# Optimization experiments

Hardware: AMD Instinct MI355X
Metric: run time of the kernel (lower is better)

Reference implementation:

```python
import jax, jax.numpy as jnp
import numpy as np

N, E, IN_DIM, HID, HEADS = 50000, 400000, 128, 64, 4
NEG_SLOPE, LN_EPS = 0.2, 1e-5


def setup_inputs() -> dict:
    key = jax.random.key(0)
    ks = jax.random.split(key, 12)
    x = jax.random.normal(ks[0], (N, IN_DIM), dtype=jnp.float32)
    edge_index = jax.random.randint(ks[1], (2, E), 0, N, dtype=jnp.int64)
    s = 1.0 / np.sqrt(HID)
    return {
        "x": x,
        "edge_index": edge_index,
        "W_gcn": jax.random.normal(ks[2], (IN_DIM, HID), dtype=jnp.float32) / np.sqrt(IN_DIM),
        "b_gcn": jnp.zeros((HID,), dtype=jnp.float32),
        "W_gat": jax.random.normal(ks[3], (HID, HEADS * HID), dtype=jnp.float32) * s,
        "att_src": jax.random.normal(ks[4], (HEADS, HID), dtype=jnp.float32) * s,
        "att_dst": jax.random.normal(ks[5], (HEADS, HID), dtype=jnp.float32) * s,
        "b_gat": jnp.zeros((HID,), dtype=jnp.float32),
        "W_patch": jax.random.normal(ks[6], (HID, HID), dtype=jnp.float32) * s,
        "b_patch": jnp.zeros((HID,), dtype=jnp.float32),
        "gamma": jnp.ones((HID,), dtype=jnp.float32),
        "beta": jnp.zeros((HID,), dtype=jnp.float32),
    }


def _forward(x, edge_index, W_gcn, b_gcn, W_gat, att_src, att_dst, b_gat,
             W_patch, b_patch, gamma, beta):
    n = x.shape[0]
    loop = jnp.arange(n, dtype=edge_index.dtype)
    src = jnp.concatenate([edge_index[0], loop])  # self-loops appended (PyG default)
    dst = jnp.concatenate([edge_index[1], loop])

    # ---- GCNConv: symmetric degree normalization + scatter-add ----
    deg = jax.ops.segment_sum(jnp.ones_like(dst, dtype=jnp.float32), dst, num_segments=n)
    dinv = jnp.where(deg > 0, jax.lax.rsqrt(deg), 0.0)
    norm = dinv[src] * dinv[dst]  # [E+N]
    xw = x @ W_gcn  # [N,HID]
    h1 = jax.ops.segment_sum(xw[src] * norm[:, None], dst, num_segments=n) + b_gcn
    h1 = jax.nn.relu(h1)

    # ---- GATConv (heads=4, concat=False -> mean over heads) ----
    z = (h1 @ W_gat).reshape(n, HEADS, HID)  # [N,H,C]
    a_s = jnp.einsum('nhc,hc->nh', z, att_src)  # [N,H]
    a_d = jnp.einsum('nhc,hc->nh', z, att_dst)
    e = jax.nn.leaky_relu(a_s[src] + a_d[dst], negative_slope=NEG_SLOPE)  # [E+N,H]
    # segment-softmax over incoming edges per destination node
    m = jax.ops.segment_max(e, dst, num_segments=n)  # [N,H]
    ex = jnp.exp(e - m[dst])
    denom = jax.ops.segment_sum(ex, dst, num_segments=n)
    alpha = ex / denom[dst]  # [E+N,H]
    agg = jax.ops.segment_sum(z[src] * alpha[:, :, None], dst, num_segments=n)  # [N,H,C]
    h2 = jax.nn.relu(agg.mean(axis=1) + b_gat)

    # ---- residual fusion + LayerNorm (dropout is identity in eval) ----
    h_patch = h1 @ W_patch + b_patch
    h = h1 + h2 + h_patch
    mu = h.mean(axis=-1, keepdims=True)
    var = h.var(axis=-1, keepdims=True)
    return (h - mu) * jax.lax.rsqrt(var + LN_EPS) * gamma + beta


def reference(x, edge_index, W_gcn, b_gcn, W_gat, att_src, att_dst, b_gat,
              W_patch, b_patch, gamma, beta):
    return _forward(x, edge_index, W_gcn, b_gcn, W_gat, att_src, att_dst, b_gat,
                    W_patch, b_patch, gamma, beta)
```

## Files before the change

kernel.cpp:

```cpp
#include <hip/hip_runtime.h>
#include <math.h>

#define IN_DIM 128
#define HID 64
#define HEADS 4
#define NEG_SLOPE 0.2f
#define LN_EPS 1e-5f
#define ECAP 512

typedef short bf16x8 __attribute__((ext_vector_type(8)));
typedef float f32x4  __attribute__((ext_vector_type(4)));

__device__ inline unsigned short f2bf(float f) {
    unsigned u = __float_as_uint(f);
    u += 0x7fffu + ((u >> 16) & 1u);
    return (unsigned short)(u >> 16);
}
__device__ inline float bf2f(unsigned short s) {
    return __uint_as_float(((unsigned)s) << 16);
}
__device__ inline float leaky(float v) { return v > 0.0f ? v : NEG_SLOPE * v; }

__global__ void k_init_all(const unsigned long long* ei, int E, int n,
                           int* flag, int* hist,
                           const float* __restrict__ Wg, const float* __restrict__ Wp,
                           const float* __restrict__ Wgcn,
                           const float* __restrict__ att_s, const float* __restrict__ att_d,
                           unsigned short* __restrict__ Wt_post,
                           unsigned short* __restrict__ Wt_xw,
                           float* __restrict__ w_s, float* __restrict__ w_d) {
    int nzb = (n + 255) >> 8;
    int t = threadIdx.x;
    if ((int)blockIdx.x < nzb) {
        int i = blockIdx.x * 256 + t;
        if (i < n) hist[i] = 0;
        if (blockIdx.x == 0) {
            __shared__ int s_bad;
            if (t == 0) s_bad = 0;
            __syncthreads();
            int lim = E < 4096 ? E : 4096;
            int bad = 0;
            for (int k = t; k < lim; k += 256)
                if (ei[k] >= (unsigned long long)n) bad = 1;
            if (bad) s_bad = 1;
            __syncthreads();
            if (t == 0) *flag = s_bad ? 0 : 1;
        }
        return;
    }
    int role = blockIdx.x - nzb;
    if (role < 14) {
        int p = role * 256 + t;
        if (p < 2560) {
            int c = p & 63, kg = p >> 6;
            bf16x8 v;
#pragma unroll
            for (int j = 0; j < 8; j++) {
                int k = kg * 8 + j;
                float f;
                if (k < 256) f = 0.25f * Wg[(size_t)(k & 63) * 256 + (k >> 6) * 64 + c];
                else         f = Wp[(size_t)(k - 256) * 64 + c];
                v[j] = (short)f2bf(f);
            }
            *(bf16x8*)(&Wt_post[(size_t)p * 8]) = v;
        } else if (p < 2560 + 1024) {
            int q = p - 2560;
            int c = q & 63, kg = q >> 6;
            bf16x8 v;
#pragma unroll
            for (int j = 0; j < 8; j++)
                v[j] = (short)f2bf(Wgcn[(size_t)(kg * 8 + j) * 64 + c]);
            *(bf16x8*)(&Wt_xw[(size_t)q * 8]) = v;
        }
    } else {
        int h = t >> 6, k = t & 63;
        float ss = 0.0f, sd = 0.0f;
        for (int c = 0; c < HID; c++) {
            float w = Wg[(size_t)k * (HEADS * HID) + h * HID + c];
            ss += w * att_s[h * HID + c];
            sd += w * att_d[h * HID + c];
        }
        w_s[h * HID + k] = ss;
        w_d[h * HID + k] = sd;
    }
}

__global__ void k_hist(const void* ei, int E, const int* flag, int* hist) {
    int i = blockIdx.x * blockDim.x + threadIdx.x;
    if (i >= E) return;
    int is64 = *flag;
    int d;
    if (is64) d = (int)((const long long*)ei)[E + i];
    else      d = ((const int*)ei)[E + i];
    atomicAdd(&hist[d], 1);
}

__global__ __launch_bounds__(256) void k_scan1(const int* __restrict__ hist,
                                               int* __restrict__ tmp,
                                               int* __restrict__ partial, int n) {
    __shared__ int s[256];
    int t = threadIdx.x, i = blockIdx.x * 256 + t;
    int v = (i < n) ? hist[i] : 0;
    s[t] = v;
    __syncthreads();
    for (int off = 1; off < 256; off <<= 1) {
        int x = (t >= off) ? s[t - off] : 0;
        __syncthreads();
        s[t] += x;
        __syncthreads();
    }
    tmp[i] = s[t] - v;
    if (t == 255) partial[blockIdx.x] = s[255];
}

__global__ __launch_bounds__(256) void k_scan_apply(const int* __restrict__ tmp,
                                                    const int* __restrict__ partial,
                                                    const int* __restrict__ hist,
                                                    int* __restrict__ row_ptr,
                                                    int* __restrict__ cursor,
                                                    float* __restrict__ dinv,
                                                    int n, int nscan) {
    __shared__ int s[256];
    __shared__ int excl_s;
    int t = threadIdx.x;
    int v = (t < nscan) ? partial[t] : 0;
    s[t] = v;
    __syncthreads();
    for (int off = 1; off < 256; off <<= 1) {
        int x = (t >= off) ? s[t - off] : 0;
        __syncthreads();
        s[t] += x;
        __syncthreads();
    }
    if (t == 0) excl_s = (blockIdx.x == 0) ? 0 : s[blockIdx.x - 1];
    __syncthreads();
    int excl = excl_s;
    int i = blockIdx.x * 256 + t;
    if (i < n) {
        int v2 = tmp[i] + excl;
        row_ptr[i] = v2;
        cursor[i] = v2;
        dinv[i] = rsqrtf((float)(hist[i] + 1));
    }
}

__global__ __launch_bounds__(256) void k_scatter_xw(const void* ei, int E,
                                                    const int* __restrict__ flag,
                                                    int* __restrict__ cursor,
                                                    int* __restrict__ col,
                                                    const float* __restrict__ x,
                                                    const unsigned short* __restrict__ Wt_g,
                                                    const float* __restrict__ dinv,
                                                    unsigned short* __restrict__ xws, int n) {
    __shared__ unsigned short Wt[16 * 64 * 8];
    int nsb = (E + 255) >> 8;
    if ((int)blockIdx.x < nsb) {
        int i = blockIdx.x * 256 + threadIdx.x;
        if (i >= E) return;
        int is64 = *flag;
        int s, d;
        if (is64) { s = (int)((const long long*)ei)[i]; d = (int)((const long long*)ei)[E + i]; }
        else      { s = ((const int*)ei)[i];            d = ((const int*)ei)[E + i]; }
        int pos = atomicAdd(&cursor[d], 1);
        col[pos] = s;
    } else {
        int bx = blockIdx.x - nsb;
        int t = threadIdx.x;
        for (int idx = t; idx < 1024; idx += 256)
            *(bf16x8*)(&Wt[idx * 8]) = *(const bf16x8*)(&Wt_g[(size_t)idx * 8]);
        __syncthreads();
        int lane = t & 63;
        int li = lane & 15, quad = lane >> 4;
        int w = t >> 6;
        int r0 = bx * 64 + w * 16;
        int rload = r0 + li; if (rload > n - 1) rload = n - 1;
        f32x4 acc[4];
#pragma unroll
        for (int i = 0; i < 4; i++) acc[i] = (f32x4){0.f, 0.f, 0.f, 0.f};
        const float* xp = x + (size_t)rload * IN_DIM + quad * 8;
#pragma unroll
        for (int ks = 0; ks < 4; ks++) {
            float4 p0 = *(const float4*)(xp + ks * 32);
            float4 p1 = *(const float4*)(xp + ks * 32 + 4);
            bf16x8 a;
            a[0] = (short)f2bf(p0.x); a[1] = (short)f2bf(p0.y);
            a[2] = (short)f2bf(p0.z); a[3] = (short)f2bf(p0.w);
            a[4] = (short)f2bf(p1.x); a[5] = (short)f2bf(p1.y);
            a[6] = (short)f2bf(p1.z); a[7] = (short)f2bf(p1.w);
            int kg = ks * 4 + quad;
#pragma unroll
            for (int tt = 0; tt < 4; tt++) {
                bf16x8 bfr = *(const bf16x8*)(&Wt[((kg * 64) + tt * 16 + li) * 8]);
                acc[tt] = __builtin_amdgcn_mfma_f32_16x16x32_bf16(a, bfr, acc[tt], 0, 0, 0);
            }
        }
#pragma unroll
        for (int reg = 0; reg < 4; reg++) {
            int r = r0 + quad * 4 + reg;
            if (r >= n) continue;
            float dv = dinv[r];
#pragma unroll
            for (int tt = 0; tt < 4; tt++)
                xws[(size_t)r * HID + tt * 16 + li] = f2bf(acc[tt][reg] * dv);
        }
    }
}

__global__ __launch_bounds__(256) void k_gcn(const int* __restrict__ col,
                                             const int* __restrict__ row_ptr,
                                             const int* __restrict__ hist,
                                             const float* __restrict__ dinv,
                                             const unsigned short* __restrict__ xws,
                                             const float* __restrict__ b,
                                             const float* __restrict__ w_s,
                                             const float* __restrict__ w_d,
                                             unsigned short* __restrict__ h1b,
                                             float4* __restrict__ a_s,
                                             float4* __restrict__ a_d, int n) {
    int t = threadIdx.x, c = t & 63;
    int d = blockIdx.x * 4 + (t >> 6);
    if (d >= n) return;
    int start = row_ptr[d], cnt = hist[d];
    float acc = bf2f(xws[(size_t)d * HID + c]);
    int k = 0;
    for (; k + 3 < cnt; k += 4) {
        int s0 = col[start + k],     s1 = col[start + k + 1];
        int s2 = col[start + k + 2], s3 = col[start + k + 3];
        float v0 = bf2f(xws[(size_t)s0 * HID + c]);
        float v1 = bf2f(xws[(size_t)s1 * HID + c]);
        float v2 = bf2f(xws[(size_t)s2 * HID + c]);
        float v3 = bf2f(xws[(size_t)s3 * HID + c]);
        acc += (v0 + v1) + (v2 + v3);
    }
    for (; k < cnt; k++) acc += bf2f(xws[(size_t)col[start + k] * HID + c]);
    float h1c = fmaxf(acc * dinv[d] + b[c], 0.0f);
    h1b[(size_t)d * HID + c] = f2bf(h1c);
    float vs0 = h1c * w_s[c],       vs1 = h1c * w_s[64 + c];
    float vs2 = h1c * w_s[128 + c], vs3 = h1c * w_s[192 + c];
    float vd0 = h1c * w_d[c],       vd1 = h1c * w_d[64 + c];
    float vd2 = h1c * w_d[128 + c], vd3 = h1c * w_d[192 + c];
    for (int o = 32; o > 0; o >>= 1) {
        vs0 += __shfl_xor(vs0, o, 64); vs1 += __shfl_xor(vs1, o, 64);
        vs2 += __shfl_xor(vs2, o, 64); vs3 += __shfl_xor(vs3, o, 64);
        vd0 += __shfl_xor(vd0, o, 64); vd1 += __shfl_xor(vd1, o, 64);
        vd2 += __shfl_xor(vd2, o, 64); vd3 += __shfl_xor(vd3, o, 64);
    }
    if (c == 0) {
        a_s[d] = make_float4(vs0, vs1, vs2, vs3);
        a_d[d] = make_float4(vd0, vd1, vd2, vd3);
    }
}

__global__ __launch_bounds__(256) void k_attn(const int* __restrict__ col,
                                              const int* __restrict__ row_ptr,
                                              const int* __restrict__ hist,
                                              const float4* __restrict__ a_s,
                                              const float4* __restrict__ a_d,
                                              const unsigned short* __restrict__ h1b,
                                              unsigned short* __restrict__ X, int n) {
    __shared__ float4 wls[ECAP];
    __shared__ int    sls[ECAP];
    __shared__ int    sb[5];
    __shared__ float4 sad[4];
    int t = threadIdx.x;
    int d0 = blockIdx.x * 4;
    if (t == 0) {
        int bptr = row_ptr[d0];
        sb[0] = bptr;
        for (int j = 0; j < 4; j++) {
            int d = d0 + j;
            bptr += (d < n) ? hist[d] : 0;
            sb[j + 1] = bptr;
        }
    }
    if (t < 4 && d0 + t < n) sad[t] = a_d[d0 + t];
    __syncthreads();
    int start0 = sb[0];
    int totc = sb[4] - start0;
    int rel1 = sb[1] - start0, rel2 = sb[2] - start0, rel3 = sb[3] - start0;
    bool fast = (totc <= ECAP);
    if (fast) {
        for (int e = t; e < totc; e += 256) {
            int s = col[start0 + e];
            int j = (e >= rel1) + (e >= rel2) + (e >= rel3);
            float4 as = a_s[s], ad = sad[j];
            float4 w;
            w.x = __expf(leaky(as.x + ad.x));
            w.y = __expf(leaky(as.y + ad.y));
            w.z = __expf(leaky(as.z + ad.z));
            w.w = __expf(leaky(as.w + ad.w));
            wls[e] = w;
            sls[e] = s;
        }
    }
    __syncthreads();
    int c = t & 63, w = t >> 6;
    int d = d0 + w;
    if (d >= n) return;
    float4 ad = sad[w];
    float4 asd = a_s[d];
    float w0 = __expf(leaky(asd.x + ad.x));
    float w1 = __expf(leaky(asd.y + ad.y));
    float w2 = __expf(leaky(asd.z + ad.z));
    float w3 = __expf(leaky(asd.w + ad.w));
    float hs = bf2f(h1b[(size_t)d * HID + c]);
    float A0 = w0 * hs, A1 = w1 * hs, A2 = w2 * hs, A3 = w3 * hs;
    float l0 = w0, l1 = w1, l2 = w2, l3 = w3;
    int lo = sb[w] - start0, hi = sb[w + 1] - start0;
    if (fast) {
        int k = lo;
        for (; k + 3 < hi; k += 4) {
            int s0 = sls[k], s1 = sls[k + 1], s2 = sls[k + 2], s3 = sls[k + 3];
            float4 e0 = wls[k], e1 = wls[k + 1], e2 = wls[k + 2], e3 = wls[k + 3];
            float hv0 = bf2f(h1b[(size_t)s0 * HID + c]);
            float hv1 = bf2f(h1b[(size_t)s1 * HID + c]);
            float hv2 = bf2f(h1b[(size_t)s2 * HID + c]);
            float hv3 = bf2f(h1b[(size_t)s3 * HID + c]);
            A0 += e0.x * hv0 + e1.x * hv1 + e2.x * hv2 + e3.x * hv3;
            A1 += e0.y * hv0 + e1.y * hv1 + e2.y * hv2 + e3.y * hv3;
            A2 += e0.z * hv0 + e1.z * hv1 + e2.z * hv2 + e3.z * hv3;
            A3 += e0.w * hv0 + e1.w * hv1 + e2.w * hv2 + e3.w * hv3;
            l0 += (e0.x + e1.x) + (e2.x + e3.x);
            l1 += (e0.y + e1.y) + (e2.y + e3.y);
            l2 += (e0.z + e1.z) + (e2.z + e3.z);
            l3 += (e0.w + e1.w) + (e2.w + e3.w);
        }
        for (; k < hi; k++) {
            int s0 = sls[k];
            float4 e0 = wls[k];
            float hv0 = bf2f(h1b[(size_t)s0 * HID + c]);
            A0 += e0.x * hv0; l0 += e0.x;
            A1 += e0.y * hv0; l1 += e0.y;
            A2 += e0.z * hv0; l2 += e0.z;
            A3 += e0.w * hv0; l3 += e0.w;
        }
    } else {
        for (int k = lo; k < hi; k++) {
            int s0 = col[start0 + k];
            float4 as = a_s[s0];
            float u0 = __expf(leaky(as.x + ad.x));
            float u1 = __expf(leaky(as.y + ad.y));
            float u2 = __expf(leaky(as.z + ad.z));
            float u3 = __expf(leaky(as.w + ad.w));
            float hv0 = bf2f(h1b[(size_t)s0 * HID + c]);
            A0 += u0 * hv0; l0 += u0;
            A1 += u1 * hv0; l1 += u1;
            A2 += u2 * hv0; l2 += u2;
            A3 += u3 * hv0; l3 += u3;
        }
    }
    size_t base = (size_t)d * 256;
    X[base + c]       = f2bf(A0 / l0);
    X[base + 64 + c]  = f2bf(A1 / l1);
    X[base + 128 + c] = f2bf(A2 / l2);
    X[base + 192 + c] = f2bf(A3 / l3);
}

__global__ __launch_bounds__(256) void k_post(const unsigned short* __restrict__ Wt_g,
                                              const unsigned short* __restrict__ X,
                                              const unsigned short* __restrict__ h1b,
                                              const float* __restrict__ bp,
                                              const float* __restrict__ bg,
                                              const float* __restrict__ gamma,
                                              const float* __restrict__ beta,
                                              float* __restrict__ out, int n) {
    __shared__ unsigned short Wt[2560 * 8];
    int t = threadIdx.x;
    for (int idx = t; idx < 2560; idx += 256)
        *(bf16x8*)(&Wt[idx * 8]) = *(const bf16x8*)(&Wt_g[(size_t)idx * 8]);
    __syncthreads();

    int lane = t & 63;
    int li = lane & 15, quad = lane >> 4;
    int w = t >> 6;
    int rbase = blockIdx.x * 128 + w * 32;

    f32x4 acc_a[2][4], acc_h[2][4];
#pragma unroll
    for (int rt = 0; rt < 2; rt++)
#pragma unroll
        for (int i = 0; i < 4; i++) {
            acc_a[rt][i] = (f32x4){0.f, 0.f, 0.f, 0.f};
            acc_h[rt][i] = (f32x4){0.f, 0.f, 0.f, 0.f};
        }
#pragma unroll
    for (int ks = 0; ks < 10; ks++) {
        int kg = ks * 4 + quad;
        bf16x8 b0 = *(const bf16x8*)(&Wt[((kg * 64) + 0 * 16 + li) * 8]);
        bf16x8 b1 = *(const bf16x8*)(&Wt[((kg * 64) + 1 * 16 + li) * 8]);
        bf16x8 b2 = *(const bf16x8*)(&Wt[((kg * 64) + 2 * 16 + li) * 8]);
        bf16x8 b3 = *(const bf16x8*)(&Wt[((kg * 64) + 3 * 16 + li) * 8]);
#pragma unroll
        for (int rt = 0; rt < 2; rt++) {
            int row = rbase + rt * 16 + li;
            bf16x8 a;
            if (ks < 8)
                a = *(const bf16x8*)(X + (size_t)row * 256 + quad * 8 + ks * 32);
            else
                a = *(const bf16x8*)(h1b + (size_t)row * HID + quad * 8 + (ks - 8) * 32);
            if (ks < 8) {
                acc_a[rt][0] = __builtin_amdgcn_mfma_f32_16x16x32_bf16(a, b0, acc_a[rt][0], 0, 0, 0);
                acc_a[rt][1] = __builtin_amdgcn_mfma_f32_16x16x32_bf16(a, b1, acc_a[rt][1], 0, 0, 0);
                acc_a[rt][2] = __builtin_amdgcn_mfma_f32_16x16x32_bf16(a, b2, acc_a[rt][2], 0, 0, 0);
                acc_a[rt][3] = __builtin_amdgcn_mfma_f32_16x16x32_bf16(a, b3, acc_a[rt][3], 0, 0, 0);
            } else {
                acc_h[rt][0] = __builtin_amdgcn_mfma_f32_16x16x32_bf16(a, b0, acc_h[rt][0], 0, 0, 0);
                acc_h[rt][1] = __builtin_amdgcn_mfma_f32_16x16x32_bf16(a, b1, acc_h[rt][1], 0, 0, 0);
                acc_h[rt][2] = __builtin_amdgcn_mfma_f32_16x16x32_bf16(a, b2, acc_h[rt][2], 0, 0, 0);
                acc_h[rt][3] = __builtin_amdgcn_mfma_f32_16x16x32_bf16(a, b3, acc_h[rt][3], 0, 0, 0);
            }
        }
    }
    float bgv[4], bpv[4], gv[4], btv[4];
#pragma unroll
    for (int tt = 0; tt < 4; tt++) {
        int c = tt * 16 + li;
        bgv[tt] = bg[c]; bpv[tt] = bp[c]; gv[tt] = gamma[c]; btv[tt] = beta[c];
    }
#pragma unroll
    for (int rt = 0; rt < 2; rt++) {
#pragma unroll
        for (int reg = 0; reg < 4; reg++) {
            int r = rbase + rt * 16 + quad * 4 + reg;
            bool ok = (r < n);
            float hv[4];
            float s1 = 0.0f, s2 = 0.0f;
#pragma unroll
            for (int tt = 0; tt < 4; tt++) {
                int c = tt * 16 + li;
                float h1c = ok ? bf2f(h1b[(size_t)r * HID + c]) : 0.0f;
                float h2 = fmaxf(acc_a[rt][tt][reg] + bgv[tt], 0.0f);
                float h = h1c + h2 + acc_h[rt][tt][reg] + bpv[tt];
                hv[tt] = h;
                s1 += h; s2 += h * h;
            }
            for (int o = 8; o > 0; o >>= 1) {
                s1 += __shfl_xor(s1, o, 64);
                s2 += __shfl_xor(s2, o, 64);
            }
            float mu = s1 * (1.0f / 64.0f);
            float var = s2 * (1.0f / 64.0f) - mu * mu;
            float rs = rsqrtf(var + LN_EPS);
            if (ok) {
#pragma unroll
                for (int tt = 0; tt < 4; tt++) {
                    int c = tt * 16 + li;
                    out[(size_t)r * HID + c] = (hv[tt] - mu) * rs * gv[tt] + btv[tt];
                }
            }
        }
    }
}

extern "C" void kernel_launch(void* const* d_in, const int* in_sizes, int n_in,
                              void* d_out, int out_size, void* d_ws, size_t ws_size,
                              hipStream_t stream) {
    int n = in_sizes[0] / IN_DIM;
    int E = in_sizes[1] / 2;

    const float* x     = (const float*)d_in[0];
    const void*  ei    = d_in[1];
    const float* W_gcn = (const float*)d_in[2];
    const float* b_gcn = (const float*)d_in[3];
    const float* W_gat = (const float*)d_in[4];
    const float* att_s = (const float*)d_in[5];
    const float* att_d = (const float*)d_in[6];
    const float* b_gat = (const float*)d_in[7];
    const float* W_p   = (const float*)d_in[8];
    const float* b_p   = (const float*)d_in[9];
    const float* gamma = (const float*)d_in[10];
    const float* beta  = (const float*)d_in[11];

    int n_pad  = ((n + 255) / 256) * 256;
    int nscan  = n_pad / 256;
    int n128   = ((n + 127) / 128) * 128;
    int nzb    = (n + 255) / 256;
    int nsb    = (E + 255) / 256;

    float* ws = (float*)d_ws;
    size_t off = 0;
    int*   flag    = (int*)(ws + off);  off += 4;
    int*   hist    = (int*)(ws + off);  off += n;
    int*   row_ptr = (int*)(ws + off);  off += n;
    int*   cursor  = (int*)(ws + off);  off += n;
    int*   tmp     = (int*)(ws + off);  off += n_pad;
    int*   partial = (int*)(ws + off);  off += 256;
    int*   colv    = (int*)(ws + off);  off += E;
    float* dinv    = ws + off;          off += n;
    float* w_s     = ws + off;          off += HEADS * HID;
    float* w_d     = ws + off;          off += HEADS * HID;
    off = (off + 3) & ~(size_t)3;
    unsigned short* Wt_post = (unsigned short*)(ws + off); off += 2560 * 8 / 2;
    unsigned short* Wt_xw   = (unsigned short*)(ws + off); off += 1024 * 8 / 2;
    unsigned short* xws = (unsigned short*)(ws + off); off += (size_t)n * HID / 2;
    off = (off + 3) & ~(size_t)3;
    unsigned short* h1b = (unsigned short*)(ws + off); off += (size_t)n128 * HID / 2;
    off = (off + 3) & ~(size_t)3;
    float4* a_sv   = (float4*)(ws + off); off += (size_t)n * 4;
    float4* a_dv   = (float4*)(ws + off); off += (size_t)n * 4;
    off = (off + 3) & ~(size_t)3;
    unsigned short* X = (unsigned short*)(ws + off); off += (size_t)n128 * 256 / 2;

    k_init_all<<<nzb + 15, 256, 0, stream>>>((const unsigned long long*)ei, E, n,
                                             flag, hist, W_gat, W_p, W_gcn,
                                             att_s, att_d, Wt_post, Wt_xw, w_s, w_d);
    k_hist<<<nsb, 256, 0, stream>>>(ei, E, flag, hist);

    k_scan1<<<nscan, 256, 0, stream>>>(hist, tmp, partial, n);
    k_scan_apply<<<nscan, 256, 0, stream>>>(tmp, partial, hist, row_ptr, cursor,
                                            dinv, n, nscan);

    k_scatter_xw<<<nsb + (n + 63) / 64, 256, 0, stream>>>(ei, E, flag, cursor,
                                                          colv, x, Wt_xw,
                                                          dinv, xws, n);

    k_gcn<<<(n + 3) / 4, 256, 0, stream>>>(colv, row_ptr, hist, dinv, xws, b_gcn,
                                           w_s, w_d, h1b, a_sv, a_dv, n);

    k_attn<<<(n + 3) / 4, 256, 0, stream>>>(colv, row_ptr, hist, a_sv, a_dv,
                                            h1b, X, n);

    k_post<<<(n + 127) / 128, 256, 0, stream>>>(Wt_post, X, h1b, b_p, b_gat,
                                                gamma, beta, (float*)d_out, n);
}
```

Baseline: 225.2 us.

## Fuse GAT attention aggregation with post-projection MFMA and LayerNorm

Merges the attention-aggregation and post-processing kernels into one. Each block aggregates 16 destination rows into a shared-memory bf16 tile, then runs the MFMA projection and LayerNorm directly from that tile, so the 256-wide intermediate X never goes through global memory. The GCN and attention gathers are restructured so each lane loads 4 contiguous bf16 values and the four 16-lane quarters of a wave walk different edges, combined with cross-quarter shuffles. The trade-offs are that attention weights are recomputed per edge instead of staged in shared memory, and the weight tile is read from global memory per block rather than cached in LDS.

```diff
diff --git a/kernel.cpp b/kernel.cpp
--- a/kernel.cpp
+++ b/kernel.cpp
@@ -6,10 +6,11 @@
 #define HEADS 4
 #define NEG_SLOPE 0.2f
 #define LN_EPS 1e-5f
-#define ECAP 512
+#define APAD 328
 
 typedef short bf16x8 __attribute__((ext_vector_type(8)));
 typedef float f32x4  __attribute__((ext_vector_type(4)));
+typedef unsigned short u16x4 __attribute__((ext_vector_type(4)));
 
 __device__ inline unsigned short f2bf(float f) {
     unsigned u = __float_as_uint(f);
@@ -217,238 +218,203 @@
                                              unsigned short* __restrict__ h1b,
                                              float4* __restrict__ a_s,
                                              float4* __restrict__ a_d, int n) {
-    int t = threadIdx.x, c = t & 63;
-    int d = blockIdx.x * 4 + (t >> 6);
+    int t = threadIdx.x;
+    int w = t >> 6, lane = t & 63, q = lane >> 4, li = lane & 15;
+    int d = blockIdx.x * 4 + w;
     if (d >= n) return;
     int start = row_ptr[d], cnt = hist[d];
-    float acc = bf2f(xws[(size_t)d * HID + c]);
-    int k = 0;
-    for (; k + 3 < cnt; k += 4) {
-        int s0 = col[start + k],     s1 = col[start + k + 1];
-        int s2 = col[start + k + 2], s3 = col[start + k + 3];
-        float v0 = bf2f(xws[(size_t)s0 * HID + c]);
-        float v1 = bf2f(xws[(size_t)s1 * HID + c]);
-        float v2 = bf2f(xws[(size_t)s2 * HID + c]);
-        float v3 = bf2f(xws[(size_t)s3 * HID + c]);
-        acc += (v0 + v1) + (v2 + v3);
-    }
-    for (; k < cnt; k++) acc += bf2f(xws[(size_t)col[start + k] * HID + c]);
-    float h1c = fmaxf(acc * dinv[d] + b[c], 0.0f);
-    h1b[(size_t)d * HID + c] = f2bf(h1c);
-    float vs0 = h1c * w_s[c],       vs1 = h1c * w_s[64 + c];
-    float vs2 = h1c * w_s[128 + c], vs3 = h1c * w_s[192 + c];
-    float vd0 = h1c * w_d[c],       vd1 = h1c * w_d[64 + c];
-    float vd2 = h1c * w_d[128 + c], vd3 = h1c * w_d[192 + c];
-    for (int o = 32; o > 0; o >>= 1) {
+    float a0, a1, a2, a3;
+    {
+        u16x4 sv = *(const u16x4*)(xws + (size_t)d * HID + li * 4);
+        float z = (q == 0) ? 1.0f : 0.0f;
+        a0 = z * bf2f(sv[0]); a1 = z * bf2f(sv[1]);
+        a2 = z * bf2f(sv[2]); a3 = z * bf2f(sv[3]);
+    }
+    int k = q;
+    int s = (k < cnt) ? col[start + k] : -1;
+    while (s >= 0) {
+        int k2 = k + 4;
+        int s2 = (k2 < cnt) ? col[start + k2] : -1;
+        u16x4 v = *(const u16x4*)(xws + (size_t)s * HID + li * 4);
+        a0 += bf2f(v[0]); a1 += bf2f(v[1]); a2 += bf2f(v[2]); a3 += bf2f(v[3]);
+        k = k2; s = s2;
+    }
+    a0 += __shfl_xor(a0, 16, 64); a1 += __shfl_xor(a1, 16, 64);
+    a2 += __shfl_xor(a2, 16, 64); a3 += __shfl_xor(a3, 16, 64);
+    a0 += __shfl_xor(a0, 32, 64); a1 += __shfl_xor(a1, 32, 64);
+    a2 += __shfl_xor(a2, 32, 64); a3 += __shfl_xor(a3, 32, 64);
+    float dv = dinv[d];
+    float4 bv = *(const float4*)(b + li * 4);
+    float h0 = fmaxf(a0 * dv + bv.x, 0.0f);
+    float h1 = fmaxf(a1 * dv + bv.y, 0.0f);
+    float h2 = fmaxf(a2 * dv + bv.z, 0.0f);
+    float h3 = fmaxf(a3 * dv + bv.w, 0.0f);
+    if (q == 0) {
+        u16x4 o;
+        o[0] = f2bf(h0); o[1] = f2bf(h1); o[2] = f2bf(h2); o[3] = f2bf(h3);
+        *(u16x4*)(h1b + (size_t)d * HID + li * 4) = o;
+    }
+    float4 u;
+    u = *(const float4*)(w_s + 0 * 64 + li * 4);
+    float vs0 = h0 * u.x + h1 * u.y + h2 * u.z + h3 * u.w;
+    u = *(const float4*)(w_s + 1 * 64 + li * 4);
+    float vs1 = h0 * u.x + h1 * u.y + h2 * u.z + h3 * u.w;
+    u = *(const float4*)(w_s + 2 * 64 + li * 4);
+    float vs2 = h0 * u.x + h1 * u.y + h2 * u.z + h3 * u.w;
+    u = *(const float4*)(w_s + 3 * 64 + li * 4);
+    float vs3 = h0 * u.x + h1 * u.y + h2 * u.z + h3 * u.w;
+    u = *(const float4*)(w_d + 0 * 64 + li * 4);
+    float vd0 = h0 * u.x + h1 * u.y + h2 * u.z + h3 * u.w;
+    u = *(const float4*)(w_d + 1 * 64 + li * 4);
+    float vd1 = h0 * u.x + h1 * u.y + h2 * u.z + h3 * u.w;
+    u = *(const float4*)(w_d + 2 * 64 + li * 4);
+    float vd2 = h0 * u.x + h1 * u.y + h2 * u.z + h3 * u.w;
+    u = *(const float4*)(w_d + 3 * 64 + li * 4);
+    float vd3 = h0 * u.x + h1 * u.y + h2 * u.z + h3 * u.w;
+#pragma unroll
+    for (int o = 1; o <= 8; o <<= 1) {
         vs0 += __shfl_xor(vs0, o, 64); vs1 += __shfl_xor(vs1, o, 64);
         vs2 += __shfl_xor(vs2, o, 64); vs3 += __shfl_xor(vs3, o, 64);
         vd0 += __shfl_xor(vd0, o, 64); vd1 += __shfl_xor(vd1, o, 64);
         vd2 += __shfl_xor(vd2, o, 64); vd3 += __shfl_xor(vd3, o, 64);
     }
-    if (c == 0) {
+    if (lane == 0) {
         a_s[d] = make_float4(vs0, vs1, vs2, vs3);
         a_d[d] = make_float4(vd0, vd1, vd2, vd3);
     }
 }
 
-__global__ __launch_bounds__(256) void k_attn(const int* __restrict__ col,
-                                              const int* __restrict__ row_ptr,
-                                              const int* __restrict__ hist,
-                                              const float4* __restrict__ a_s,
-                                              const float4* __restrict__ a_d,
-                                              const unsigned short* __restrict__ h1b,
-                                              unsigned short* __restrict__ X, int n) {
-    __shared__ float4 wls[ECAP];
-    __shared__ int    sls[ECAP];
-    __shared__ int    sb[5];
-    __shared__ float4 sad[4];
+__global__ __launch_bounds__(256) void k_attn_post(
+        const int* __restrict__ col, const int* __restrict__ row_ptr,
+        const int* __restrict__ hist,
+        const float4* __restrict__ a_s, const float4* __restrict__ a_d,
+        const unsigned short* __restrict__ h1b,
+        const unsigned short* __restrict__ Wt_g,
+        const float* __restrict__ bp, const float* __restrict__ bg,
+        const float* __restrict__ gamma, const float* __restrict__ beta,
+        float* __restrict__ out, int n) {
+    __shared__ unsigned short Atile[16 * APAD];
+    __shared__ float hbuf[16 * 68];
     int t = threadIdx.x;
-    int d0 = blockIdx.x * 4;
-    if (t == 0) {
-        int bptr = row_ptr[d0];
-        sb[0] = bptr;
-        for (int j = 0; j < 4; j++) {
-            int d = d0 + j;
-            bptr += (d < n) ? hist[d] : 0;
-            sb[j + 1] = bptr;
-        }
-    }
-    if (t < 4 && d0 + t < n) sad[t] = a_d[d0 + t];
+    int w = t >> 6, lane = t & 63, q = lane >> 4, li = lane & 15;
+    int rowbase = blockIdx.x * 16;
+
+    for (int j = 0; j < 4; j++) {
+        int r = w * 4 + j;
+        int d = rowbase + r;
+        if (d >= n) {
+            for (int c = lane; c < 320; c += 64) Atile[r * APAD + c] = 0;
+            continue;
+        }
+        int start = row_ptr[d], cnt = hist[d];
+        float4 ad = a_d[d];
+        float4 asd = a_s[d];
+        u16x4 sv = *(const u16x4*)(h1b + (size_t)d * HID + li * 4);
+        float e0 = __expf(leaky(asd.x + ad.x));
+        float e1 = __expf(leaky(asd.y + ad.y));
+        float e2 = __expf(leaky(asd.z + ad.z));
+        float e3 = __expf(leaky(asd.w + ad.w));
+        float z = (q == 0) ? 1.0f : 0.0f;
+        float f0 = bf2f(sv[0]), f1 = bf2f(sv[1]), f2 = bf2f(sv[2]), f3 = bf2f(sv[3]);
+        f32x4 A0 = {z * e0 * f0, z * e0 * f1, z * e0 * f2, z * e0 * f3};
+        f32x4 A1 = {z * e1 * f0, z * e1 * f1, z * e1 * f2, z * e1 * f3};
+        f32x4 A2 = {z * e2 * f0, z * e2 * f1, z * e2 * f2, z * e2 * f3};
+        f32x4 A3 = {z * e3 * f0, z * e3 * f1, z * e3 * f2, z * e3 * f3};
+        float l0 = z * e0, l1 = z * e1, l2 = z * e2, l3 = z * e3;
+        int k = q;
+        int s = (k < cnt) ? col[start + k] : -1;
+        while (s >= 0) {
+            int k2 = k + 4;
+            int s2 = (k2 < cnt) ? col[start + k2] : -1;
+            float4 as = a_s[s];
+            u16x4 hv = *(const u16x4*)(h1b + (size_t)s * HID + li * 4);
+            float w0 = __expf(leaky(as.x + ad.x));
+            float w1 = __expf(leaky(as.y + ad.y));
+            float w2 = __expf(leaky(as.z + ad.z));
+            float w3 = __expf(leaky(as.w + ad.w));
+            float g0 = bf2f(hv[0]), g1 = bf2f(hv[1]);
+            float g2 = bf2f(hv[2]), g3 = bf2f(hv[3]);
+            A0[0] += w0 * g0; A0[1] += w0 * g1; A0[2] += w0 * g2; A0[3] += w0 * g3;
+            A1[0] += w1 * g0; A1[1] += w1 * g1; A1[2] += w1 * g2; A1[3] += w1 * g3;
+            A2[0] += w2 * g0; A2[1] += w2 * g1; A2[2] += w2 * g2; A2[3] += w2 * g3;
+            A3[0] += w3 * g0; A3[1] += w3 * g1; A3[2] += w3 * g2; A3[3] += w3 * g3;
+            l0 += w0; l1 += w1; l2 += w2; l3 += w3;
+            k = k2; s = s2;
+        }
+#pragma unroll
+        for (int c4 = 0; c4 < 4; c4++) {
+            A0[c4] += __shfl_xor(A0[c4], 16, 64);
+            A1[c4] += __shfl_xor(A1[c4], 16, 64);
+            A2[c4] += __shfl_xor(A2[c4], 16, 64);
+            A3[c4] += __shfl_xor(A3[c4], 16, 64);
+        }
+        l0 += __shfl_xor(l0, 16, 64); l1 += __shfl_xor(l1, 16, 64);
+        l2 += __shfl_xor(l2, 16, 64); l3 += __shfl_xor(l3, 16, 64);
+#pragma unroll
+        for (int c4 = 0; c4 < 4; c4++) {
+            A0[c4] += __shfl_xor(A0[c4], 32, 64);
+            A1[c4] += __shfl_xor(A1[c4], 32, 64);
+            A2[c4] += __shfl_xor(A2[c4], 32, 64);
+            A3[c4] += __shfl_xor(A3[c4], 32, 64);
+        }
+        l0 += __shfl_xor(l0, 32, 64); l1 += __shfl_xor(l1, 32, 64);
+        l2 += __shfl_xor(l2, 32, 64); l3 += __shfl_xor(l3, 32, 64);
+        f32x4 Aq; float lq;
+        if (q == 0)      { Aq = A0; lq = l0; }
+        else if (q == 1) { Aq = A1; lq = l1; }
+        else if (q == 2) { Aq = A2; lq = l2; }
+        else             { Aq = A3; lq = l3; }
+        float inv = 1.0f / lq;
+        u16x4 o;
+        o[0] = f2bf(Aq[0] * inv); o[1] = f2bf(Aq[1] * inv);
+        o[2] = f2bf(Aq[2] * inv); o[3] = f2bf(Aq[3] * inv);
+        *(u16x4*)(&Atile[r * APAD + q * 64 + li * 4]) = o;
+        if (q == 0) *(u16x4*)(&Atile[r * APAD + 256 + li * 4]) = sv;
+    }
     __syncthreads();
-    int start0 = sb[0];
-    int totc = sb[4] - start0;
-    int rel1 = sb[1] - start0, rel2 = sb[2] - start0, rel3 = sb[3] - start0;
-    bool fast = (totc <= ECAP);
-    if (fast) {
-        for (int e = t; e < totc; e += 256) {
-            int s = col[start0 + e];
-            int j = (e >= rel1) + (e >= rel2) + (e >= rel3);
-            float4 as = a_s[s], ad = sad[j];
-            float4 w;
-            w.x = __expf(leaky(as.x + ad.x));
-            w.y = __expf(leaky(as.y + ad.y));
-            w.z = __expf(leaky(as.z + ad.z));
-            w.w = __expf(leaky(as.w + ad.w));
-            wls[e] = w;
-            sls[e] = s;
-        }
+
+    f32x4 acc_a = {0.f, 0.f, 0.f, 0.f}, acc_h = {0.f, 0.f, 0.f, 0.f};
+#pragma unroll
+    for (int ks = 0; ks < 10; ks++) {
+        int kg = ks * 4 + q;
+        bf16x8 a = *(const bf16x8*)(&Atile[li * APAD + ks * 32 + q * 8]);
+        bf16x8 bb = *(const bf16x8*)(&Wt_g[(size_t)(kg * 64 + w * 16 + li) * 8]);
+        if (ks < 8) acc_a = __builtin_amdgcn_mfma_f32_16x16x32_bf16(a, bb, acc_a, 0, 0, 0);
+        else        acc_h = __builtin_amdgcn_mfma_f32_16x16x32_bf16(a, bb, acc_h, 0, 0, 0);
+    }
+    int cc = w * 16 + li;
+    float bgv = bg[cc], bpv = bp[cc];
+#pragma unroll
+    for (int reg = 0; reg < 4; reg++) {
+        int r = q * 4 + reg;
+        float h1c = bf2f(Atile[r * APAD + 256 + cc]);
+        float h2v = fmaxf(acc_a[reg] + bgv, 0.0f);
+        hbuf[r * 68 + cc] = h1c + h2v + acc_h[reg] + bpv;
     }
     __syncthreads();
-    int c = t & 63, w = t >> 6;
-    int d = d0 + w;
-    if (d >= n) return;
-    float4 ad = sad[w];
-    float4 asd = a_s[d];
-    float w0 = __expf(leaky(asd.x + ad.x));
-    float w1 = __expf(leaky(asd.y + ad.y));
-    float w2 = __expf(leaky(asd.z + ad.z));
-    float w3 = __expf(leaky(asd.w + ad.w));
-    float hs = bf2f(h1b[(size_t)d * HID + c]);
-    float A0 = w0 * hs, A1 = w1 * hs, A2 = w2 * hs, A3 = w3 * hs;
-    float l0 = w0, l1 = w1, l2 = w2, l3 = w3;
-    int lo = sb[w] - start0, hi = sb[w + 1] - start0;
-    if (fast) {
-        int k = lo;
-        for (; k + 3 < hi; k += 4) {
-            int s0 = sls[k], s1 = sls[k + 1], s2 = sls[k + 2], s3 = sls[k + 3];
-            float4 e0 = wls[k], e1 = wls[k + 1], e2 = wls[k + 2], e3 = wls[k + 3];
-            float hv0 = bf2f(h1b[(size_t)s0 * HID + c]);
-            float hv1 = bf2f(h1b[(size_t)s1 * HID + c]);
-            float hv2 = bf2f(h1b[(size_t)s2 * HID + c]);
-            float hv3 = bf2f(h1b[(size_t)s3 * HID + c]);
-            A0 += e0.x * hv0 + e1.x * hv1 + e2.x * hv2 + e3.x * hv3;
-            A1 += e0.y * hv0 + e1.y * hv1 + e2.y * hv2 + e3.y * hv3;
-            A2 += e0.z * hv0 + e1.z * hv1 + e2.z * hv2 + e3.z * hv3;
-            A3 += e0.w * hv0 + e1.w * hv1 + e2.w * hv2 + e3.w * hv3;
-            l0 += (e0.x + e1.x) + (e2.x + e3.x);
-            l1 += (e0.y + e1.y) + (e2.y + e3.y);
-            l2 += (e0.z + e1.z) + (e2.z + e3.z);
-            l3 += (e0.w + e1.w) + (e2.w + e3.w);
-        }
-        for (; k < hi; k++) {
-            int s0 = sls[k];
-            float4 e0 = wls[k];
-            float hv0 = bf2f(h1b[(size_t)s0 * HID + c]);
-            A0 += e0.x * hv0; l0 += e0.x;
-            A1 += e0.y * hv0; l1 += e0.y;
-            A2 += e0.z * hv0; l2 += e0.z;
-            A3 += e0.w * hv0; l3 += e0.w;
-        }
-    } else {
-        for (int k = lo; k < hi; k++) {
-            int s0 = col[start0 + k];
-            float4 as = a_s[s0];
-            float u0 = __expf(leaky(as.x + ad.x));
-            float u1 = __expf(leaky(as.y + ad.y));
-            float u2 = __expf(leaky(as.z + ad.z));
-            float u3 = __expf(leaky(as.w + ad.w));
-            float hv0 = bf2f(h1b[(size_t)s0 * HID + c]);
-            A0 += u0 * hv0; l0 += u0;
-            A1 += u1 * hv0; l1 += u1;
-            A2 += u2 * hv0; l2 += u2;
-            A3 += u3 * hv0; l3 += u3;
-        }
-    }
-    size_t base = (size_t)d * 256;
-    X[base + c]       = f2bf(A0 / l0);
-    X[base + 64 + c]  = f2bf(A1 / l1);
-    X[base + 128 + c] = f2bf(A2 / l2);
-    X[base + 192 + c] = f2bf(A3 / l3);
-}
-
-__global__ __launch_bounds__(256) void k_post(const unsigned short* __restrict__ Wt_g,
-                                              const unsigned short* __restrict__ X,
-                                              const unsigned short* __restrict__ h1b,
-                                              const float* __restrict__ bp,
-                                              const float* __restrict__ bg,
-                                              const float* __restrict__ gamma,
-                                              const float* __restrict__ beta,
-                                              float* __restrict__ out, int n) {
-    __shared__ unsigned short Wt[2560 * 8];
-    int t = threadIdx.x;
-    for (int idx = t; idx < 2560; idx += 256)
-        *(bf16x8*)(&Wt[idx * 8]) = *(const bf16x8*)(&Wt_g[(size_t)idx * 8]);
-    __syncthreads();
-
-    int lane = t & 63;
-    int li = lane & 15, quad = lane >> 4;
-    int w = t >> 6;
-    int rbase = blockIdx.x * 128 + w * 32;
-
-    f32x4 acc_a[2][4], acc_h[2][4];
-#pragma unroll
-    for (int rt = 0; rt < 2; rt++)
-#pragma unroll
-        for (int i = 0; i < 4; i++) {
-            acc_a[rt][i] = (f32x4){0.f, 0.f, 0.f, 0.f};
-            acc_h[rt][i] = (f32x4){0.f, 0.f, 0.f, 0.f};
-        }
-#pragma unroll
-    for (int ks = 0; ks < 10; ks++) {
-        int kg = ks * 4 + quad;
-        bf16x8 b0 = *(const bf16x8*)(&Wt[((kg * 64) + 0 * 16 + li) * 8]);
-        bf16x8 b1 = *(const bf16x8*)(&Wt[((kg * 64) + 1 * 16 + li) * 8]);
-        bf16x8 b2 = *(const bf16x8*)(&Wt[((kg * 64) + 2 * 16 + li) * 8]);
-        bf16x8 b3 = *(const bf16x8*)(&Wt[((kg * 64) + 3 * 16 + li) * 8]);
-#pragma unroll
-        for (int rt = 0; rt < 2; rt++) {
-            int row = rbase + rt * 16 + li;
-            bf16x8 a;
-            if (ks < 8)
-                a = *(const bf16x8*)(X + (size_t)row * 256 + quad * 8 + ks * 32);
-            else
-                a = *(const bf16x8*)(h1b + (size_t)row * HID + quad * 8 + (ks - 8) * 32);
-            if (ks < 8) {
-                acc_a[rt][0] = __builtin_amdgcn_mfma_f32_16x16x32_bf16(a, b0, acc_a[rt][0], 0, 0, 0);
-                acc_a[rt][1] = __builtin_amdgcn_mfma_f32_16x16x32_bf16(a, b1, acc_a[rt][1], 0, 0, 0);
-                acc_a[rt][2] = __builtin_amdgcn_mfma_f32_16x16x32_bf16(a, b2, acc_a[rt][2], 0, 0, 0);
-                acc_a[rt][3] = __builtin_amdgcn_mfma_f32_16x16x32_bf16(a, b3, acc_a[rt][3], 0, 0, 0);
-            } else {
-                acc_h[rt][0] = __builtin_amdgcn_mfma_f32_16x16x32_bf16(a, b0, acc_h[rt][0], 0, 0, 0);
-                acc_h[rt][1] = __builtin_amdgcn_mfma_f32_16x16x32_bf16(a, b1, acc_h[rt][1], 0, 0, 0);
-                acc_h[rt][2] = __builtin_amdgcn_mfma_f32_16x16x32_bf16(a, b2, acc_h[rt][2], 0, 0, 0);
-                acc_h[rt][3] = __builtin_amdgcn_mfma_f32_16x16x32_bf16(a, b3, acc_h[rt][3], 0, 0, 0);
-            }
-        }
-    }
-    float bgv[4], bpv[4], gv[4], btv[4];
-#pragma unroll
-    for (int tt = 0; tt < 4; tt++) {
-        int c = tt * 16 + li;
-        bgv[tt] = bg[c]; bpv[tt] = bp[c]; gv[tt] = gamma[c]; btv[tt] = beta[c];
-    }
-#pragma unroll
-    for (int rt = 0; rt < 2; rt++) {
-#pragma unroll
-        for (int reg = 0; reg < 4; reg++) {
-            int r = rbase + rt * 16 + quad * 4 + reg;
-            bool ok = (r < n);
-            float hv[4];
-            float s1 = 0.0f, s2 = 0.0f;
-#pragma unroll
-            for (int tt = 0; tt < 4; tt++) {
-                int c = tt * 16 + li;
-                float h1c = ok ? bf2f(h1b[(size_t)r * HID + c]) : 0.0f;
-                float h2 = fmaxf(acc_a[rt][tt][reg] + bgv[tt], 0.0f);
-                float h = h1c + h2 + acc_h[rt][tt][reg] + bpv[tt];
-                hv[tt] = h;
-                s1 += h; s2 += h * h;
-            }
-            for (int o = 8; o > 0; o >>= 1) {
-                s1 += __shfl_xor(s1, o, 64);
-                s2 += __shfl_xor(s2, o, 64);
-            }
-            float mu = s1 * (1.0f / 64.0f);
-            float var = s2 * (1.0f / 64.0f) - mu * mu;
-            float rs = rsqrtf(var + LN_EPS);
-            if (ok) {
-#pragma unroll
-                for (int tt = 0; tt < 4; tt++) {
-                    int c = tt * 16 + li;
-                    out[(size_t)r * HID + c] = (hv[tt] - mu) * rs * gv[tt] + btv[tt];
-                }
-            }
-        }
+
+    int row = t >> 4, lj = t & 15;
+    f32x4 hv4 = *(const f32x4*)(&hbuf[row * 68 + lj * 4]);
+    float s1 = (hv4[0] + hv4[1]) + (hv4[2] + hv4[3]);
+    float s2 = (hv4[0] * hv4[0] + hv4[1] * hv4[1]) + (hv4[2] * hv4[2] + hv4[3] * hv4[3]);
+#pragma unroll
+    for (int o = 1; o <= 8; o <<= 1) {
+        s1 += __shfl_xor(s1, o, 64);
+        s2 += __shfl_xor(s2, o, 64);
+    }
+    float mu = s1 * (1.0f / 64.0f);
+    float var = s2 * (1.0f / 64.0f) - mu * mu;
+    float rs = rsqrtf(var + LN_EPS);
+    int rg = rowbase + row;
+    if (rg < n) {
+        float4 g4 = *(const float4*)(gamma + lj * 4);
+        float4 b4 = *(const float4*)(beta + lj * 4);
+        float4 ov;
+        ov.x = (hv4[0] - mu) * rs * g4.x + b4.x;
+        ov.y = (hv4[1] - mu) * rs * g4.y + b4.y;
+        ov.z = (hv4[2] - mu) * rs * g4.z + b4.z;
+        ov.w = (hv4[3] - mu) * rs * g4.w + b4.w;
+        *(float4*)(out + (size_t)rg * HID + lj * 4) = ov;
     }
 }
 
@@ -498,8 +464,6 @@
     off = (off + 3) & ~(size_t)3;
     float4* a_sv   = (float4*)(ws + off); off += (size_t)n * 4;
     float4* a_dv   = (float4*)(ws + off); off += (size_t)n * 4;
-    off = (off + 3) & ~(size_t)3;
-    unsigned short* X = (unsigned short*)(ws + off); off += (size_t)n128 * 256 / 2;
 
     k_init_all<<<nzb + 15, 256, 0, stream>>>((const unsigned long long*)ei, E, n,
                                              flag, hist, W_gat, W_p, W_gcn,
@@ -517,9 +481,7 @@
     k_gcn<<<(n + 3) / 4, 256, 0, stream>>>(colv, row_ptr, hist, dinv, xws, b_gcn,
                                            w_s, w_d, h1b, a_sv, a_dv, n);
 
-    k_attn<<<(n + 3) / 4, 256, 0, stream>>>(colv, row_ptr, hist, a_sv, a_dv,
-                                            h1b, X, n);
-
-    k_post<<<(n + 127) / 128, 256, 0, stream>>>(Wt_post, X, h1b, b_p, b_gat,
-                                                gamma, beta, (float*)d_out, n);
-}
+    k_attn_post<<<(n + 15) / 16, 256, 0, stream>>>(colv, row_ptr, hist, a_sv, a_dv,
+                                                   h1b, Wt_post, b_p, b_gat,
+                                                   gamma, beta, (float*)d_out, n);
+}
```

New measurement: 214.9 us. 1.05x faster.
